# Optimization experiments

Measured on AMD Instinct MI355X. Metric: run time of the kernel, lower is better.

Reference implementation:

```python
import jax, jax.numpy as jnp
import numpy as np

HIDDEN = 1024
HEADS = 16
HEAD_DIM = HIDDEN // HEADS
SCALE = 1.0 / (HEAD_DIM ** 0.5)


def setup_inputs() -> dict:
    key = jax.random.key(0)
    k1, k2, k3 = jax.random.split(key, 3)
    B, S = 2, 2048
    x = jax.random.normal(k1, (B, S, HIDDEN), dtype=jnp.float32)
    # torch Linear weights: (out_features, in_features), y = x @ W.T
    qkv_w = jax.random.normal(k2, (3 * HIDDEN, HIDDEN), dtype=jnp.float32) * (HIDDEN ** -0.5)
    out_w = jax.random.normal(k3, (HIDDEN, HIDDEN), dtype=jnp.float32) * (HIDDEN ** -0.5)
    return {"x": x, "qkv_w": qkv_w, "out_w": out_w}


def reference(x, qkv_w, out_w):
    B, S, H = x.shape
    qkv = jnp.einsum('bsh,oh->bso', x, qkv_w)  # [B,S,3H]
    q, k, v = jnp.split(qkv, 3, axis=-1)
    def heads(t):
        return t.reshape(B, S, HEADS, HEAD_DIM).transpose(0, 2, 1, 3)  # [B,nh,S,hd]
    q, k, v = heads(q), heads(k), heads(v)
    scores = jnp.einsum('bhqd,bhkd->bhqk', q, k) * SCALE  # [B,nh,S,S]
    attn = jax.nn.softmax(scores, axis=-1)
    out = jnp.einsum('bhqk,bhkd->bhqd', attn, v)  # [B,nh,S,hd]
    out = out.transpose(0, 2, 1, 3).reshape(B, S, H)
    return jnp.einsum('bsh,oh->bso', out, out_w)
```

## Files before the change

kernel.cpp:

```cpp
#include <hip/hip_runtime.h>
#include <hip/hip_bf16.h>

#define BB 2
#define SS 2048
#define HH 1024
#define NH 16
#define HD 64
#define MM (BB * SS)
#define N_QKV (3 * HH)
#define KK HH

typedef __attribute__((ext_vector_type(8))) short short8;
typedef __attribute__((ext_vector_type(4))) float floatx4;
typedef __attribute__((ext_vector_type(16))) float floatx16;

#define MFMA16(a, b, c) __builtin_amdgcn_mfma_f32_16x16x32_bf16(a, b, c, 0, 0, 0)
#define MFMA32(a, b, c) __builtin_amdgcn_mfma_f32_32x32x16_bf16(a, b, c, 0, 0, 0)

__device__ __forceinline__ unsigned short f2bf(float f) {
  unsigned int u = __builtin_bit_cast(unsigned int, f);
  u += 0x7FFFu + ((u >> 16) & 1u);
  return (unsigned short)(u >> 16);
}

__device__ __forceinline__ float fexp2(float x) {
#if __has_builtin(__builtin_amdgcn_exp2f)
  return __builtin_amdgcn_exp2f(x);
#else
  float r; asm("v_exp_f32 %0, %1" : "=v"(r) : "v"(x)); return r;
#endif
}

__device__ __forceinline__ void gl_lds16(const unsigned short* g, unsigned short* l) {
  __builtin_amdgcn_global_load_lds((const __attribute__((address_space(1))) void*)g,
                                   (__attribute__((address_space(3))) void*)l,
                                   16, 0, 0);
}

#define N4X (MM * HH / 4)
#define N4Q (N_QKV * KK / 4)
#define N4O (HH * KK / 4)
__global__ __launch_bounds__(256) void cast3_f32_bf16(const float* __restrict__ x,
                                                      const float* __restrict__ qw,
                                                      const float* __restrict__ ow,
                                                      unsigned short* __restrict__ xb,
                                                      unsigned short* __restrict__ qwb,
                                                      unsigned short* __restrict__ owb) {
  int i = blockIdx.x * blockDim.x + threadIdx.x;
  const float* src; unsigned short* dst; int idx;
  if (i < N4X) { src = x; dst = xb; idx = i; }
  else if (i < N4X + N4Q) { src = qw; dst = qwb; idx = i - N4X; }
  else { src = ow; dst = owb; idx = i - N4X - N4Q; }
  float4 f = ((const float4*)src)[idx];
  ushort4 u;
  u.x = f2bf(f.x); u.y = f2bf(f.y); u.z = f2bf(f.z); u.w = f2bf(f.w);
  ((ushort4*)dst)[idx] = u;
}

__global__ __launch_bounds__(256) void gemm_qkv(const unsigned short* __restrict__ A,
                                                const unsigned short* __restrict__ W,
                                                unsigned short* __restrict__ qb,
                                                unsigned short* __restrict__ kb,
                                                unsigned short* __restrict__ vtb) {
  __shared__ __attribute__((aligned(16))) unsigned short As[128 * 32];
  __shared__ __attribute__((aligned(16))) unsigned short Bs[128 * 32];
  const int tid = threadIdx.x;
  const int wave = tid >> 6, lane = tid & 63;
  const int quad = lane >> 4, lc = lane & 15;
  const int m0 = blockIdx.y * 128, n0 = blockIdx.x * 128;
  const int wm = (wave >> 1) * 64, wn = (wave & 1) * 64;

  floatx4 acc[4][4];
#pragma unroll
  for (int i = 0; i < 4; i++)
#pragma unroll
    for (int j = 0; j < 4; j++) acc[i][j] = (floatx4){0.f, 0.f, 0.f, 0.f};

  const unsigned short* Ag = A + (size_t)(m0 + (tid >> 2)) * KK + (tid & 3) * 8;
  const unsigned short* Bg = W + (size_t)(n0 + (tid >> 2)) * KK + (tid & 3) * 8;
  unsigned short* AsW = As + wave * 512;
  unsigned short* BsW = Bs + wave * 512;

  for (int k0 = 0; k0 < KK; k0 += 32) {
    gl_lds16(Ag + k0, AsW);
    gl_lds16(Ag + k0 + (size_t)64 * KK, AsW + 2048);
    gl_lds16(Bg + k0, BsW);
    gl_lds16(Bg + k0 + (size_t)64 * KK, BsW + 2048);
    __syncthreads();
    short8 af[4], bf[4];
#pragma unroll
    for (int i = 0; i < 4; i++) {
      af[i] = *(const short8*)(As + (wm + i * 16 + lc) * 32 + quad * 8);
      bf[i] = *(const short8*)(Bs + (wn + i * 16 + lc) * 32 + quad * 8);
    }
#pragma unroll
    for (int i = 0; i < 4; i++)
#pragma unroll
      for (int j = 0; j < 4; j++) acc[i][j] = MFMA16(af[i], bf[j], acc[i][j]);
    __syncthreads();
  }

  const float QSCALE = 0.125f * 1.44269504f;
#pragma unroll
  for (int j = 0; j < 4; j++) {
    int n = n0 + wn + j * 16 + lc;
#pragma unroll
    for (int i = 0; i < 4; i++) {
      int mbase = m0 + wm + i * 16 + quad * 4;
      int b = mbase >> 11;
      int s0 = mbase & 2047;
      if (n < HH) {
        int h = n >> 6, d = n & 63;
#pragma unroll
        for (int r = 0; r < 4; r++)
          qb[(((size_t)(b * NH + h) * SS + s0 + r) * HD) + d] = f2bf(acc[i][j][r] * QSCALE);
      } else if (n < 2 * HH) {
        int n2 = n - HH; int h = n2 >> 6, d = n2 & 63;
#pragma unroll
        for (int r = 0; r < 4; r++)
          kb[(((size_t)(b * NH + h) * SS + s0 + r) * HD) + d] = f2bf(acc[i][j][r]);
      } else {
        int n2 = n - 2 * HH; int h = n2 >> 6, d = n2 & 63;
        ushort4 p;
        p.x = f2bf(acc[i][j][0]); p.y = f2bf(acc[i][j][1]);
        p.z = f2bf(acc[i][j][2]); p.w = f2bf(acc[i][j][3]);
        *(ushort4*)(vtb + ((size_t)(b * NH + h) * HD + d) * SS + s0) = p;
      }
    }
  }
}

__device__ __forceinline__ int co(int row, int c16) {
  return row * 64 + ((c16 ^ ((row ^ (row >> 3)) & 7)) << 3);
}

__global__ __launch_bounds__(256, 2) void attn_kernel(const unsigned short* __restrict__ qg,
                                                      const unsigned short* __restrict__ kg,
                                                      const unsigned short* __restrict__ vtg,
                                                      unsigned short* __restrict__ og) {
  __shared__ __attribute__((aligned(16))) unsigned short Qs[128 * 64];
  __shared__ __attribute__((aligned(16))) unsigned short Ks[64 * 64];
  __shared__ __attribute__((aligned(16))) unsigned short Vs[64 * 64];
  __shared__ __attribute__((aligned(16))) unsigned short Ps[4 * 32 * 64];

  const int tid = threadIdx.x;
  const int w = tid >> 6, lane = tid & 63;
  const int hl = lane >> 5, c = lane & 31;
  const int q0 = blockIdx.x * 128;
  const int head = blockIdx.y, b = blockIdx.z;

  const unsigned short* qbase = qg + (size_t)(b * NH + head) * SS * HD;
  const unsigned short* kbase = kg + (size_t)(b * NH + head) * SS * HD;
  const unsigned short* vbase = vtg + (size_t)(b * NH + head) * HD * SS;

  {
    int row = tid >> 3, cc = tid & 7;
#pragma unroll
    for (int s = 0; s < 4; s++)
      *(uint4*)(Qs + co(row + 32 * s, cc)) =
          *(const uint4*)(qbase + (size_t)(q0 + row + 32 * s) * HD + cc * 8);
  }

  const int frow = tid >> 3, fc = tid & 7;
  uint4 k0r = *(const uint4*)(kbase + (size_t)frow * HD + fc * 8);
  uint4 k1r = *(const uint4*)(kbase + (size_t)(frow + 32) * HD + fc * 8);
  uint4 v0r = *(const uint4*)(vbase + (size_t)frow * SS + fc * 8);
  uint4 v1r = *(const uint4*)(vbase + (size_t)(frow + 32) * SS + fc * 8);

  floatx16 oacc0, oacc1, lacc;
#pragma unroll
  for (int i = 0; i < 16; i++) { oacc0[i] = 0.f; oacc1[i] = 0.f; lacc[i] = 0.f; }

  short8 ones;
#pragma unroll
  for (int i = 0; i < 8; i++) ones[i] = (short)0x3F80;

  short8 qa[4];
  unsigned short* pw = Ps + w * 2048;

  for (int kt = 0; kt < SS; kt += 64) {
    __syncthreads();
    *(uint4*)(Ks + co(frow, fc)) = k0r;
    *(uint4*)(Ks + co(frow + 32, fc)) = k1r;
    *(uint4*)(Vs + co(frow, fc)) = v0r;
    *(uint4*)(Vs + co(frow + 32, fc)) = v1r;
    if (kt + 64 < SS) {
      k0r = *(const uint4*)(kbase + (size_t)(kt + 64 + frow) * HD + fc * 8);
      k1r = *(const uint4*)(kbase + (size_t)(kt + 96 + frow) * HD + fc * 8);
      v0r = *(const uint4*)(vbase + (size_t)frow * SS + kt + 64 + fc * 8);
      v1r = *(const uint4*)(vbase + (size_t)(frow + 32) * SS + kt + 64 + fc * 8);
    }
    __syncthreads();

    if (kt == 0) {
#pragma unroll
      for (int ks = 0; ks < 4; ks++)
        qa[ks] = *(const short8*)(Qs + co(w * 32 + c, ks * 2 + hl));
    }

    floatx16 sacc0, sacc1;
#pragma unroll
    for (int i = 0; i < 16; i++) { sacc0[i] = 0.f; sacc1[i] = 0.f; }
#pragma unroll
    for (int ks = 0; ks < 4; ks++) {
      short8 kb0 = *(const short8*)(Ks + co(2 * c + 0, ks * 2 + hl));
      short8 kb1 = *(const short8*)(Ks + co(2 * c + 1, ks * 2 + hl));
      sacc0 = MFMA32(qa[ks], kb0, sacc0);
      sacc1 = MFMA32(qa[ks], kb1, sacc1);
    }

#pragma unroll
    for (int r = 0; r < 16; r++) {
      int prow = (r & 3) + 8 * (r >> 2) + 4 * hl;
      unsigned int u0 = __builtin_bit_cast(unsigned int, fexp2(sacc0[r])) + 0x8000u;
      unsigned int u1 = __builtin_bit_cast(unsigned int, fexp2(sacc1[r])) + 0x8000u;
      unsigned int u = __builtin_amdgcn_perm(u1, u0, 0x07060302u);
      *(unsigned int*)(pw + co(prow, c >> 2) + (c & 3) * 2) = u;
    }

    short8 pa[4];
#pragma unroll
    for (int ks = 0; ks < 4; ks++)
      pa[ks] = *(const short8*)(pw + co(c, ks * 2 + hl));
#pragma unroll
    for (int ks = 0; ks < 4; ks++) {
      short8 vb0 = *(const short8*)(Vs + co(c, ks * 2 + hl));
      short8 vb1 = *(const short8*)(Vs + co(32 + c, ks * 2 + hl));
      oacc0 = MFMA32(pa[ks], vb0, oacc0);
      oacc1 = MFMA32(pa[ks], vb1, oacc1);
      lacc = MFMA32(pa[ks], ones, lacc);
    }
  }

#pragma unroll
  for (int r = 0; r < 16; r++) {
    int prow = (r & 3) + 8 * (r >> 2) + 4 * hl;
    size_t row = (size_t)(b * SS + q0 + w * 32 + prow);
    float inv = 1.0f / lacc[r];
    og[row * HH + head * 64 + c] = f2bf(oacc0[r] * inv);
    og[row * HH + head * 64 + 32 + c] = f2bf(oacc1[r] * inv);
  }
}

__global__ __launch_bounds__(256) void gemm_out(const unsigned short* __restrict__ A,
                                                const unsigned short* __restrict__ W,
                                                float* __restrict__ C) {
  __shared__ __attribute__((aligned(16))) unsigned short As[128 * 32];
  __shared__ __attribute__((aligned(16))) unsigned short Bs[64 * 32];
  const int tid = threadIdx.x;
  const int wave = tid >> 6, lane = tid & 63;
  const int quad = lane >> 4, lc = lane & 15;
  const int m0 = blockIdx.y * 128, n0 = blockIdx.x * 64;
  const int wm = (wave >> 1) * 64, wn = (wave & 1) * 32;

  floatx4 acc[4][2];
#pragma unroll
  for (int i = 0; i < 4; i++)
#pragma unroll
    for (int j = 0; j < 2; j++) acc[i][j] = (floatx4){0.f, 0.f, 0.f, 0.f};

  const unsigned short* Ag = A + (size_t)(m0 + (tid >> 2)) * KK + (tid & 3) * 8;
  const unsigned short* Bg = W + (size_t)(n0 + (tid >> 2)) * KK + (tid & 3) * 8;

  for (int k0 = 0; k0 < KK; k0 += 32) {
    gl_lds16(Ag + k0, As + wave * 512);
    gl_lds16(Ag + k0 + (size_t)64 * KK, As + 2048 + wave * 512);
    gl_lds16(Bg + k0, Bs + wave * 512);
    __syncthreads();
    short8 af[4], bf[2];
#pragma unroll
    for (int i = 0; i < 4; i++)
      af[i] = *(const short8*)(As + (wm + i * 16 + lc) * 32 + quad * 8);
#pragma unroll
    for (int j = 0; j < 2; j++)
      bf[j] = *(const short8*)(Bs + (wn + j * 16 + lc) * 32 + quad * 8);
#pragma unroll
    for (int i = 0; i < 4; i++)
#pragma unroll
      for (int j = 0; j < 2; j++) acc[i][j] = MFMA16(af[i], bf[j], acc[i][j]);
    __syncthreads();
  }

#pragma unroll
  for (int i = 0; i < 4; i++)
#pragma unroll
    for (int j = 0; j < 2; j++) {
      int m = m0 + wm + i * 16 + quad * 4;
      int n = n0 + wn + j * 16 + lc;
#pragma unroll
      for (int r = 0; r < 4; r++) C[(size_t)(m + r) * HH + n] = acc[i][j][r];
    }
}

extern "C" void kernel_launch(void* const* d_in, const int* in_sizes, int n_in,
                              void* d_out, int out_size, void* d_ws, size_t ws_size,
                              hipStream_t stream) {
  const float* x = (const float*)d_in[0];
  const float* qkv_w = (const float*)d_in[1];
  const float* out_w = (const float*)d_in[2];
  float* out = (float*)d_out;

  char* ws = (char*)d_ws;
  unsigned short* x_bf   = (unsigned short*)(ws + 0);
  unsigned short* qkw_bf = (unsigned short*)(ws + 8388608);
  unsigned short* otw_bf = (unsigned short*)(ws + 14680064);
  unsigned short* qb     = (unsigned short*)(ws + 16777216);
  unsigned short* kb     = (unsigned short*)(ws + 25165824);
  unsigned short* vtb    = (unsigned short*)(ws + 33554432);
  unsigned short* ao     = (unsigned short*)(ws + 41943040);

  cast3_f32_bf16<<<dim3((N4X + N4Q + N4O) / 256), dim3(256), 0, stream>>>(
      x, qkv_w, out_w, x_bf, qkw_bf, otw_bf);
  gemm_qkv<<<dim3(N_QKV / 128, MM / 128), dim3(256), 0, stream>>>(x_bf, qkw_bf, qb, kb, vtb);
  attn_kernel<<<dim3(SS / 128, NH, BB), dim3(256), 0, stream>>>(qb, kb, vtb, ao);
  gemm_out<<<dim3(HH / 64, MM / 128), dim3(256), 0, stream>>>(ao, otw_bf, out);
}
```

Baseline: 197.2 us.

## Compute transposed S in attention to keep P in registers, skip LDS round-trip

The attention kernel now computes S^T = K·Q^T, so each lane's accumulator holds a contiguous run of keys for one query. The exponentiated scores can then be packed straight into bf16 B-operands for the P·V MFMA with no trip through shared memory. The Ps buffer is removed and all LDS is merged into one array, which lowers shared memory per block and may raise occupancy. The output is staged through LDS so it can be written with 16-byte coalesced stores instead of scattered 2-byte ones. In exchange, V fragments are now read from LDS as split 8-byte loads, and the extra output staging adds a final synchronisation.

```diff
diff --git a/kernel.cpp b/kernel.cpp
--- a/kernel.cpp
+++ b/kernel.cpp
@@ -29,6 +29,12 @@
 #else
   float r; asm("v_exp_f32 %0, %1" : "=v"(r) : "v"(x)); return r;
 #endif
+}
+
+__device__ __forceinline__ unsigned int pack2(float lo, float hi) {
+  unsigned int a = __builtin_bit_cast(unsigned int, lo) + 0x8000u;
+  unsigned int b = __builtin_bit_cast(unsigned int, hi) + 0x8000u;
+  return __builtin_amdgcn_perm(b, a, 0x07060302u);
 }
 
 __device__ __forceinline__ void gl_lds16(const unsigned short* g, unsigned short* l) {
@@ -138,10 +144,10 @@
                                                       const unsigned short* __restrict__ kg,
                                                       const unsigned short* __restrict__ vtg,
                                                       unsigned short* __restrict__ og) {
-  __shared__ __attribute__((aligned(16))) unsigned short Qs[128 * 64];
-  __shared__ __attribute__((aligned(16))) unsigned short Ks[64 * 64];
-  __shared__ __attribute__((aligned(16))) unsigned short Vs[64 * 64];
-  __shared__ __attribute__((aligned(16))) unsigned short Ps[4 * 32 * 64];
+  __shared__ __attribute__((aligned(16))) unsigned short Sall[16384];
+  unsigned short* Qs = Sall;
+  unsigned short* Ks = Sall + 8192;
+  unsigned short* Vs = Sall + 12288;
 
   const int tid = threadIdx.x;
   const int w = tid >> 6, lane = tid & 63;
@@ -176,7 +182,6 @@
   for (int i = 0; i < 8; i++) ones[i] = (short)0x3F80;
 
   short8 qa[4];
-  unsigned short* pw = Ps + w * 2048;
 
   for (int kt = 0; kt < SS; kt += 64) {
     __syncthreads();
@@ -203,42 +208,62 @@
     for (int i = 0; i < 16; i++) { sacc0[i] = 0.f; sacc1[i] = 0.f; }
 #pragma unroll
     for (int ks = 0; ks < 4; ks++) {
-      short8 kb0 = *(const short8*)(Ks + co(2 * c + 0, ks * 2 + hl));
-      short8 kb1 = *(const short8*)(Ks + co(2 * c + 1, ks * 2 + hl));
-      sacc0 = MFMA32(qa[ks], kb0, sacc0);
-      sacc1 = MFMA32(qa[ks], kb1, sacc1);
-    }
-
-#pragma unroll
-    for (int r = 0; r < 16; r++) {
-      int prow = (r & 3) + 8 * (r >> 2) + 4 * hl;
-      unsigned int u0 = __builtin_bit_cast(unsigned int, fexp2(sacc0[r])) + 0x8000u;
-      unsigned int u1 = __builtin_bit_cast(unsigned int, fexp2(sacc1[r])) + 0x8000u;
-      unsigned int u = __builtin_amdgcn_perm(u1, u0, 0x07060302u);
-      *(unsigned int*)(pw + co(prow, c >> 2) + (c & 3) * 2) = u;
-    }
-
-    short8 pa[4];
-#pragma unroll
-    for (int ks = 0; ks < 4; ks++)
-      pa[ks] = *(const short8*)(pw + co(c, ks * 2 + hl));
-#pragma unroll
-    for (int ks = 0; ks < 4; ks++) {
-      short8 vb0 = *(const short8*)(Vs + co(c, ks * 2 + hl));
-      short8 vb1 = *(const short8*)(Vs + co(32 + c, ks * 2 + hl));
-      oacc0 = MFMA32(pa[ks], vb0, oacc0);
-      oacc1 = MFMA32(pa[ks], vb1, oacc1);
-      lacc = MFMA32(pa[ks], ones, lacc);
-    }
-  }
-
-#pragma unroll
-  for (int r = 0; r < 16; r++) {
-    int prow = (r & 3) + 8 * (r >> 2) + 4 * hl;
-    size_t row = (size_t)(b * SS + q0 + w * 32 + prow);
-    float inv = 1.0f / lacc[r];
-    og[row * HH + head * 64 + c] = f2bf(oacc0[r] * inv);
-    og[row * HH + head * 64 + 32 + c] = f2bf(oacc1[r] * inv);
+      short8 ka0 = *(const short8*)(Ks + co(c, ks * 2 + hl));
+      short8 ka1 = *(const short8*)(Ks + co(32 + c, ks * 2 + hl));
+      sacc0 = MFMA32(ka0, qa[ks], sacc0);
+      sacc1 = MFMA32(ka1, qa[ks], sacc1);
+    }
+
+    short8 pb[4];
+#pragma unroll
+    for (int kb = 0; kb < 4; kb++) {
+      const floatx16& s = (kb < 2) ? sacc0 : sacc1;
+      int base = (kb & 1) * 8;
+      unsigned int u0 = pack2(fexp2(s[base + 0]), fexp2(s[base + 1]));
+      unsigned int u1 = pack2(fexp2(s[base + 2]), fexp2(s[base + 3]));
+      unsigned int u2 = pack2(fexp2(s[base + 4]), fexp2(s[base + 5]));
+      unsigned int u3 = pack2(fexp2(s[base + 6]), fexp2(s[base + 7]));
+      uint4 u = {u0, u1, u2, u3};
+      pb[kb] = __builtin_bit_cast(short8, u);
+    }
+
+#pragma unroll
+    for (int kb = 0; kb < 4; kb++) {
+      uint2 lo0 = *(const uint2*)(Vs + co(c, 2 * kb) + 4 * hl);
+      uint2 hi0 = *(const uint2*)(Vs + co(c, 2 * kb + 1) + 4 * hl);
+      uint4 a0 = {lo0.x, lo0.y, hi0.x, hi0.y};
+      short8 va0 = __builtin_bit_cast(short8, a0);
+      uint2 lo1 = *(const uint2*)(Vs + co(32 + c, 2 * kb) + 4 * hl);
+      uint2 hi1 = *(const uint2*)(Vs + co(32 + c, 2 * kb + 1) + 4 * hl);
+      uint4 a1 = {lo1.x, lo1.y, hi1.x, hi1.y};
+      short8 va1 = __builtin_bit_cast(short8, a1);
+      oacc0 = MFMA32(va0, pb[kb], oacc0);
+      oacc1 = MFMA32(va1, pb[kb], oacc1);
+      lacc = MFMA32(ones, pb[kb], lacc);
+    }
+  }
+
+  __syncthreads();
+  unsigned short* sc = Sall + w * 2176;
+  float inv = 1.0f / lacc[0];
+#pragma unroll
+  for (int t = 0; t < 8; t++) {
+    int d0 = ((2 * t) & 3) + 8 * (t >> 1) + 4 * hl;
+    *(unsigned int*)(sc + c * 68 + d0) = pack2(oacc0[2 * t] * inv, oacc0[2 * t + 1] * inv);
+    *(unsigned int*)(sc + c * 68 + 32 + d0) = pack2(oacc1[2 * t] * inv, oacc1[2 * t + 1] * inv);
+  }
+  {
+    int ql = lane >> 1, hf = lane & 1;
+    size_t row = (size_t)(b * SS + q0 + w * 32 + ql);
+    unsigned short* dst = og + row * HH + head * 64 + hf * 32;
+    const unsigned short* srcp = sc + ql * 68 + hf * 32;
+#pragma unroll
+    for (int s = 0; s < 4; s++) {
+      uint2 a = *(const uint2*)(srcp + s * 8);
+      uint2 bq = *(const uint2*)(srcp + s * 8 + 4);
+      uint4 v = {a.x, a.y, bq.x, bq.y};
+      *(uint4*)(dst + s * 8) = v;
+    }
   }
 }
 
```

New measurement: 193.3 us. 1.02x faster.
